# Optimization experiments

Measured on AMD Instinct MI355X. Metric: run time of the kernel, lower is better.

## Reference

```python
import jax, jax.numpy as jnp
import numpy as np
from jax import lax

EPS = 1e-5
B, T, IN, H, D = 16, 512, 128, 256, 8


def setup_inputs() -> dict:
    key = jax.random.key(0)
    ks = jax.random.split(key, 9)
    s = 0.05  # small init to keep tanh unsaturated
    f32 = jnp.float32
    return {
        "y": jax.random.normal(ks[0], (B, T, IN), f32),
        "W_ih": jax.random.normal(ks[1], (H, IN), f32) * s,
        "W_hh": jax.random.normal(ks[2], (H, H), f32) * s,
        "b_ih": jax.random.normal(ks[3], (H,), f32) * s,
        "b_hh": jax.random.normal(ks[4], (H,), f32) * s,
        "W_mean": jax.random.normal(ks[5], (D, H), f32) * s,
        "b_mean": jax.random.normal(ks[6], (D,), f32) * s,
        "W_bd": jax.random.normal(ks[7], (2 * D, H), f32) * s,
        "b_bd": jax.random.normal(ks[8], (2 * D,), f32) * s,
    }


def _forward(y, W_ih, W_hh, b_ih, b_hh, W_mean, b_mean, W_bd, b_bd):
    # --- single-layer unidirectional tanh RNN (torch nn.RNN, batch_first) ---
    x_proj = jnp.einsum("bti,hi->bth", y, W_ih) + b_ih  # [B,T,H]

    def step(h, xt):
        h_new = jnp.tanh(xt + h @ W_hh.T + b_hh)
        return h_new, h_new

    h0 = jnp.zeros((y.shape[0], W_hh.shape[0]), y.dtype)
    _, hs = lax.scan(step, h0, jnp.swapaxes(x_proj, 0, 1))  # [T,B,H]
    enc = jnp.swapaxes(hs, 0, 1)  # [B,T,H]

    mean = enc @ W_mean.T + b_mean  # [B,T,D]
    bd = enc @ W_bd.T + b_bd        # [B,T,2D]

    d = mean.shape[-1]
    t = bd.shape[1]
    diag_e = bd[:, :, :d]        # [B,T,D]  main-diag factor elems
    off_e = bd[:, :-1, d:]       # [B,T-1,D] super-diag factor elems

    a2 = diag_e ** 2
    b2 = jnp.concatenate([jnp.zeros_like(off_e[:, :1]), off_e ** 2], axis=1)  # [B,T,D]
    ab = diag_e[:, :-1] * off_e  # [B,T-1,D]

    main = jnp.swapaxes(a2 + b2, 1, 2) + EPS  # [B,D,T]  (eps*I folded into diag)
    supd = jnp.swapaxes(ab, 1, 2)             # [B,D,T-1]

    i = jnp.arange(t)
    j = jnp.arange(t - 1)
    prec = jnp.zeros((bd.shape[0], d, t, t), bd.dtype)  # [B,D,T,T]
    prec = prec.at[:, :, i, i].set(main)
    prec = prec.at[:, :, j, j + 1].set(supd)
    prec = prec.at[:, :, j + 1, j].set(supd)
    return mean, prec


def reference(y, W_ih, W_hh, b_ih, b_hh, W_mean, b_mean, W_bd, b_bd):
    # Returns the parameters of the D per-dim MultivariateNormal posteriors:
    # mean [B,T,D] and tridiagonal precision matrices [B,D,T,T].
    return _forward(y, W_ih, W_hh, b_ih, b_hh, W_mean, b_mean, W_bd, b_bd)
```

## Files before the change

### kernel.cpp

```cpp
#include <hip/hip_runtime.h>
#include <math.h>

#define BB 16
#define TT 512
#define IND 128
#define HH 256
#define DD 8
#define EPSF 1e-5f

typedef _Float16 h2_t __attribute__((ext_vector_type(2)));

__device__ __forceinline__ float fast_tanh(float x) {
    x = fminf(fmaxf(x, -15.f), 15.f);
    const float e = __expf(2.f * x);
    return __fdividef(e - 1.f, e + 1.f);
}

__device__ __forceinline__ float dpp_xor1(float x) {
    int i = __builtin_bit_cast(int, x);
    i = __builtin_amdgcn_update_dpp(i, i, 0xB1, 0xF, 0xF, true);
    return __builtin_bit_cast(float, i);
}
__device__ __forceinline__ float dpp_xor2(float x) {
    int i = __builtin_bit_cast(int, x);
    i = __builtin_amdgcn_update_dpp(i, i, 0x4E, 0xF, 0xF, true);
    return __builtin_bit_cast(float, i);
}

__global__ __launch_bounds__(512, 4) void xproj_kernel(
    const float* __restrict__ y, const float* __restrict__ W_ih,
    const float* __restrict__ b_ih, const float* __restrict__ b_hh,
    float* __restrict__ xp)
{
    __shared__ __align__(16) float ylds[IND];
    const int tid = threadIdx.x;
    const int j = tid >> 1;
    const int k4 = (tid & 1) * 4;

    float4 w[16];
    const float* wr = W_ih + (size_t)j * IND + k4;
#pragma unroll
    for (int i = 0; i < 16; ++i) w[i] = *(const float4*)(wr + i * 8);
#pragma unroll
    for (int i = 0; i < 16; ++i)
        asm volatile("" : "+v"(w[i].x), "+v"(w[i].y), "+v"(w[i].z), "+v"(w[i].w));
    const float bias = b_ih[j] + b_hh[j];

    const int row0 = blockIdx.x * 16;
    for (int r = 0; r < 16; ++r) {
        const int row = row0 + r;
        if (tid < IND / 4) ((float4*)ylds)[tid] = ((const float4*)(y + (size_t)row * IND))[tid];
        __syncthreads();
        float a0 = 0.f, a1 = 0.f, a2 = 0.f, a3 = 0.f;
#pragma unroll
        for (int i = 0; i < 16; ++i) {
            const float4 hv = *(const float4*)(ylds + i * 8 + k4);
            a0 = fmaf(hv.x, w[i].x, a0);
            a1 = fmaf(hv.y, w[i].y, a1);
            a2 = fmaf(hv.z, w[i].z, a2);
            a3 = fmaf(hv.w, w[i].w, a3);
        }
        float acc = (a0 + a1) + (a2 + a3);
        acc += __shfl_xor(acc, 1);
        if ((tid & 1) == 0) xp[(size_t)row * HH + j] = acc + bias;
        __syncthreads();
    }
}

__global__ __launch_bounds__(256, 2) void scan_fill_kernel(
    const float* __restrict__ xp, const float* __restrict__ W_hh,
    float* __restrict__ enc, float* __restrict__ prec)
{
    if (blockIdx.x >= BB) {
        const size_t n4 = (size_t)BB * DD * TT * TT / 4;
        const float4 z = make_float4(0.f, 0.f, 0.f, 0.f);
        float4* p4 = (float4*)prec;
        size_t idx = (size_t)(blockIdx.x - BB) * blockDim.x + threadIdx.x;
        const size_t stride = (size_t)(gridDim.x - BB) * blockDim.x;
        for (; idx < n4; idx += stride) p4[idx] = z;
        return;
    }

    const int b = blockIdx.x;
    const int tid = threadIdx.x;
    const int j0 = tid >> 2;
    const int k  = tid & 3;
    const int jw = j0 + 64 * k;

    __shared__ __align__(16) char hbufA[4 * 144];
    __shared__ __align__(16) char hbufB[4 * 144];

    h2_t w[4][32];
#pragma unroll
    for (int m = 0; m < 4; ++m) {
        const float* wr = W_hh + (size_t)(j0 + 64 * m) * HH + (size_t)k * 64;
#pragma unroll
        for (int q = 0; q < 16; ++q) {
            const float4 f = ((const float4*)wr)[q];
            h2_t v0; v0.x = (_Float16)f.x; v0.y = (_Float16)f.y;
            h2_t v1; v1.x = (_Float16)f.z; v1.y = (_Float16)f.w;
            w[m][2 * q]     = v0;
            w[m][2 * q + 1] = v1;
        }
    }
#pragma unroll
    for (int m = 0; m < 4; ++m)
#pragma unroll
        for (int i = 0; i < 32; ++i) {
            int tmp = __builtin_bit_cast(int, w[m][i]);
            asm volatile("" : "+v"(tmp));
            w[m][i] = __builtin_bit_cast(h2_t, tmp);
        }

    if (tid < 128) {
        const int m = 2 * tid;
        h2_t z; z.x = (_Float16)0.f; z.y = (_Float16)0.f;
        *(h2_t*)(hbufA + (m >> 6) * 144 + (m & 63) * 2) = z;
    }

    const float* xpb = xp + (size_t)b * TT * HH;
    float* encb = enc + (size_t)b * TT * HH;

    float xbuf[4];
#pragma unroll
    for (int s = 0; s < 4; ++s) xbuf[s] = xpb[(size_t)s * HH + jw];

    __syncthreads();

    const char* hrd = hbufA;
    char* hwr = hbufB;

    for (int tb = 0; tb < TT; tb += 4) {
#pragma unroll
        for (int s = 0; s < 4; ++s) {
            const int t = tb + s;
            const float xc = xbuf[s];
            {
                const int tp = (t + 4 < TT) ? (t + 4) : (TT - 1);
                xbuf[s] = xpb[(size_t)tp * HH + jw];
            }

            float a0 = 0.f, a1 = 0.f, a2 = 0.f, a3 = 0.f;
            const float4* hp = (const float4*)(hrd + k * 144);
#pragma unroll
            for (int i = 0; i < 8; ++i) {
                union { float4 f4; h2_t h[4]; } u;
                u.f4 = hp[i];
#pragma unroll
                for (int q = 0; q < 4; ++q) {
                    a0 = __builtin_amdgcn_fdot2(u.h[q], w[0][4 * i + q], a0, false);
                    a1 = __builtin_amdgcn_fdot2(u.h[q], w[1][4 * i + q], a1, false);
                    a2 = __builtin_amdgcn_fdot2(u.h[q], w[2][4 * i + q], a2, false);
                    a3 = __builtin_amdgcn_fdot2(u.h[q], w[3][4 * i + q], a3, false);
                }
            }
            a0 += dpp_xor1(a0); a0 += dpp_xor2(a0);
            a1 += dpp_xor1(a1); a1 += dpp_xor2(a1);
            a2 += dpp_xor1(a2); a2 += dpp_xor2(a2);
            a3 += dpp_xor1(a3); a3 += dpp_xor2(a3);
            const float p = (k & 1) ? ((k & 2) ? a3 : a1) : ((k & 2) ? a2 : a0);
            const float hn = fast_tanh(xc + p);

            encb[(size_t)t * HH + jw] = hn;
            *(_Float16*)(hwr + k * 144 + j0 * 2) = (_Float16)hn;

            asm volatile("s_waitcnt lgkmcnt(0)\n\ts_barrier" ::: "memory");
            const char* tmp = hrd; hrd = hwr; hwr = (char*)tmp;
        }
    }
}

__global__ __launch_bounds__(256) void head_kernel(
    const float* __restrict__ enc,
    const float* __restrict__ W_mean, const float* __restrict__ b_mean,
    const float* __restrict__ W_bd, const float* __restrict__ b_bd,
    float* __restrict__ mean_out, float* __restrict__ prec)
{
    const int b = blockIdx.x >> 6;
    const int t0 = (blockIdx.x & 63) * 8;
    __shared__ __align__(16) float erow[9][HH];
    __shared__ float vals[8][32];

    const int tid = threadIdx.x;
    {
        const float4* src = (const float4*)(enc + ((size_t)b * TT + t0) * HH - HH);
        float4* dst = (float4*)erow;
        for (int i = tid; i < 9 * (HH / 4); i += 256) dst[i] = src[i];
    }

    const int g = tid >> 3, m = tid & 7;
    const float* wrow;
    float bias;
    if (g < 8)       { wrow = W_mean + (size_t)g * HH;      bias = b_mean[g]; }
    else if (g < 24) { wrow = W_bd + (size_t)(g - 8) * HH;  bias = b_bd[g - 8]; }
    else             { wrow = W_bd + (size_t)(g - 16) * HH; bias = b_bd[g - 16]; }

    float4 wv[8];
#pragma unroll
    for (int i = 0; i < 8; ++i) wv[i] = ((const float4*)wrow)[m * 8 + i];

    __syncthreads();

    for (int r = 0; r < 8; ++r) {
        const float* src = (g >= 24) ? erow[r] : erow[r + 1];
        float acc = 0.f;
#pragma unroll
        for (int i = 0; i < 8; ++i) {
            const float4 hv = ((const float4*)src)[m * 8 + i];
            acc += wv[i].x * hv.x + wv[i].y * hv.y + wv[i].z * hv.z + wv[i].w * hv.w;
        }
        acc += __shfl_xor(acc, 1);
        acc += __shfl_xor(acc, 2);
        acc += __shfl_xor(acc, 4);
        if (m == 0) vals[r][g] = acc + bias;
    }
    __syncthreads();

    const int r = tid >> 5, s = tid & 31;
    const int t = t0 + r;
    if (s < DD) {
        mean_out[((size_t)b * TT + t) * DD + s] = vals[r][s];
    } else if (s < 2 * DD) {
        const int d = s - DD;
        const float diag = vals[r][8 + d];
        const float off  = vals[r][16 + d];
        const float offp = (t > 0) ? vals[r][24 + d] : 0.f;
        const size_t rowbase = (((size_t)b * DD + d) * TT + t) * TT;
        prec[rowbase + t] = diag * diag + offp * offp + EPSF;
        if (t < TT - 1) {
            const float sv = diag * off;
            prec[rowbase + t + 1] = sv;
            prec[(((size_t)b * DD + d) * TT + (t + 1)) * TT + t] = sv;
        }
    }
}

extern "C" void kernel_launch(void* const* d_in, const int* in_sizes, int n_in,
                              void* d_out, int out_size, void* d_ws, size_t ws_size,
                              hipStream_t stream) {
    const float* y      = (const float*)d_in[0];
    const float* W_ih   = (const float*)d_in[1];
    const float* W_hh   = (const float*)d_in[2];
    const float* b_ih   = (const float*)d_in[3];
    const float* b_hh   = (const float*)d_in[4];
    const float* W_mean = (const float*)d_in[5];
    const float* b_mean = (const float*)d_in[6];
    const float* W_bd   = (const float*)d_in[7];
    const float* b_bd   = (const float*)d_in[8];

    float* out  = (float*)d_out;
    float* mean = out;
    float* prec = out + (size_t)BB * TT * DD;

    float* xp  = (float*)d_ws;
    float* enc = xp + (size_t)BB * TT * HH;

    xproj_kernel<<<512, 512, 0, stream>>>(y, W_ih, b_ih, b_hh, xp);
    scan_fill_kernel<<<1008, 256, 0, stream>>>(xp, W_hh, enc, prec);
    head_kernel<<<1024, 256, 0, stream>>>(enc, W_mean, b_mean, W_bd, b_bd, mean, prec);
}
```

Measured before the change: 410.9 us.

## Split recurrent matvec across 8 lanes per row group with 512-thread scan blocks

The sequential RNN scan block grows from 256 to 512 threads. Each output group's K=256 reduction is now split across 8 lanes instead of 4, which halves the per-thread fdot2 chain and the register-resident W_hh slice, and adds a cross-lane shfl_xor(4) stage to the reduction. Only half the lanes write results. The fill blocks also become 512 threads, doubling the zeroing parallelism. The cost is a barrier across 8 waves instead of 4 per timestep, plus the extra shuffle latency on the critical path.

```diff
diff --git a/kernel.cpp b/kernel.cpp
--- a/kernel.cpp
+++ b/kernel.cpp
@@ -9,6 +9,7 @@
 #define EPSF 1e-5f
 
 typedef _Float16 h2_t __attribute__((ext_vector_type(2)));
+typedef float f32x4 __attribute__((ext_vector_type(4)));
 
 __device__ __forceinline__ float fast_tanh(float x) {
     x = fminf(fmaxf(x, -15.f), 15.f);
@@ -67,46 +68,47 @@
     }
 }
 
-__global__ __launch_bounds__(256, 2) void scan_fill_kernel(
+__global__ __launch_bounds__(512, 2) void scan_fill_kernel(
     const float* __restrict__ xp, const float* __restrict__ W_hh,
     float* __restrict__ enc, float* __restrict__ prec)
 {
     if (blockIdx.x >= BB) {
         const size_t n4 = (size_t)BB * DD * TT * TT / 4;
-        const float4 z = make_float4(0.f, 0.f, 0.f, 0.f);
-        float4* p4 = (float4*)prec;
+        const f32x4 z = {0.f, 0.f, 0.f, 0.f};
+        f32x4* p4 = (f32x4*)prec;
         size_t idx = (size_t)(blockIdx.x - BB) * blockDim.x + threadIdx.x;
         const size_t stride = (size_t)(gridDim.x - BB) * blockDim.x;
         for (; idx < n4; idx += stride) p4[idx] = z;
         return;
     }
 
-    const int b = blockIdx.x;
+    const int b   = blockIdx.x;
     const int tid = threadIdx.x;
-    const int j0 = tid >> 2;
-    const int k  = tid & 3;
-    const int jw = j0 + 64 * k;
+    const int g   = tid >> 3;
+    const int k   = tid & 7;
+    const int kk  = k & 3;
+    const int jw  = g + 64 * kk;
+    const bool act = (k < 4);
 
     __shared__ __align__(16) char hbufA[4 * 144];
     __shared__ __align__(16) char hbufB[4 * 144];
 
-    h2_t w[4][32];
+    h2_t w[4][16];
 #pragma unroll
     for (int m = 0; m < 4; ++m) {
-        const float* wr = W_hh + (size_t)(j0 + 64 * m) * HH + (size_t)k * 64;
-#pragma unroll
-        for (int q = 0; q < 16; ++q) {
-            const float4 f = ((const float4*)wr)[q];
-            h2_t v0; v0.x = (_Float16)f.x; v0.y = (_Float16)f.y;
-            h2_t v1; v1.x = (_Float16)f.z; v1.y = (_Float16)f.w;
-            w[m][2 * q]     = v0;
-            w[m][2 * q + 1] = v1;
+        const float* wr = W_hh + (size_t)(g + 64 * m) * HH + (size_t)k * 32;
+#pragma unroll
+        for (int i = 0; i < 16; ++i) {
+            h2_t v;
+            v.x = (_Float16)wr[2 * i];
+            v.y = (_Float16)wr[2 * i + 1];
+            w[m][i] = v;
         }
     }
 #pragma unroll
     for (int m = 0; m < 4; ++m)
 #pragma unroll
-        for (int i = 0; i < 32; ++i) {
+        for (int i = 0; i < 16; ++i) {
             int tmp = __builtin_bit_cast(int, w[m][i]);
             asm volatile("" : "+v"(tmp));
             w[m][i] = __builtin_bit_cast(h2_t, tmp);
@@ -118,8 +120,8 @@
         *(h2_t*)(hbufA + (m >> 6) * 144 + (m & 63) * 2) = z;
     }
 
-    const float* xpb = xp + (size_t)b * TT * HH;
-    float* encb = enc + (size_t)b * TT * HH;
+    const float* xpb  = xp  + (size_t)b * TT * HH;
+    float*       encb = enc + (size_t)b * TT * HH;
 
     float xbuf[4];
 #pragma unroll
@@ -130,44 +132,47 @@
     const char* hrd = hbufA;
     char* hwr = hbufB;
 
+#define SCAN_STEP(TSTEP, S)                                                       \
+    {                                                                             \
+        const int t_ = (TSTEP);                                                   \
+        const float xc = xbuf[S];                                                 \
+        const int tp_ = (t_ + 4 < TT) ? t_ + 4 : TT - 1;                          \
+        xbuf[S] = xpb[(size_t)tp_ * HH + jw];                                     \
+        float a0 = 0.f, a1 = 0.f, a2 = 0.f, a3 = 0.f;                             \
+        const float4* hp = (const float4*)(hrd + (k >> 1) * 144 + (k & 1) * 64);  \
+        _Pragma("unroll")                                                         \
+        for (int i = 0; i < 4; ++i) {                                             \
+            union { float4 f4; h2_t h[4]; } u;                                    \
+            u.f4 = hp[i];                                                         \
+            _Pragma("unroll")                                                     \
+            for (int e = 0; e < 4; ++e) {                                         \
+                a0 = __builtin_amdgcn_fdot2(u.h[e], w[0][4 * i + e], a0, false);  \
+                a1 = __builtin_amdgcn_fdot2(u.h[e], w[1][4 * i + e], a1, false);  \
+                a2 = __builtin_amdgcn_fdot2(u.h[e], w[2][4 * i + e], a2, false);  \
+                a3 = __builtin_amdgcn_fdot2(u.h[e], w[3][4 * i + e], a3, false);  \
+            }                                                                     \
+        }                                                                         \
+        a0 += dpp_xor1(a0); a0 += dpp_xor2(a0); a0 += __shfl_xor(a0, 4);          \
+        a1 += dpp_xor1(a1); a1 += dpp_xor2(a1); a1 += __shfl_xor(a1, 4);          \
+        a2 += dpp_xor1(a2); a2 += dpp_xor2(a2); a2 += __shfl_xor(a2, 4);          \
+        a3 += dpp_xor1(a3); a3 += dpp_xor2(a3); a3 += __shfl_xor(a3, 4);          \
+        const float p = (kk & 1) ? ((kk & 2) ? a3 : a1) : ((kk & 2) ? a2 : a0);   \
+        const float hn = fast_tanh(xc + p);                                       \
+        if (act) {                                                                \
+            encb[(size_t)t_ * HH + jw] = hn;                                      \
+            *(_Float16*)(hwr + kk * 144 + g * 2) = (_Float16)hn;                  \
+        }                                                                         \
+        asm volatile("s_waitcnt lgkmcnt(0)\n\ts_barrier" ::: "memory");           \
+        { const char* tmp_ = hrd; hrd = hwr; hwr = (char*)tmp_; }                 \
+    }
+
     for (int tb = 0; tb < TT; tb += 4) {
-#pragma unroll
-        for (int s = 0; s < 4; ++s) {
-            const int t = tb + s;
-            const float xc = xbuf[s];
-            {
-                const int tp = (t + 4 < TT) ? (t + 4) : (TT - 1);
-                xbuf[s] = xpb[(size_t)tp * HH + jw];
-            }
-
-            float a0 = 0.f, a1 = 0.f, a2 = 0.f, a3 = 0.f;
-            const float4* hp = (const float4*)(hrd + k * 144);
-#pragma unroll
-            for (int i = 0; i < 8; ++i) {
-                union { float4 f4; h2_t h[4]; } u;
-                u.f4 = hp[i];
-#pragma unroll
-                for (int q = 0; q < 4; ++q) {
-                    a0 = __builtin_amdgcn_fdot2(u.h[q], w[0][4 * i + q], a0, false);
-                    a1 = __builtin_amdgcn_fdot2(u.h[q], w[1][4 * i + q], a1, false);
-                    a2 = __builtin_amdgcn_fdot2(u.h[q], w[2][4 * i + q], a2, false);
-                    a3 = __builtin_amdgcn_fdot2(u.h[q], w[3][4 * i + q], a3, false);
-                }
-            }
-            a0 += dpp_xor1(a0); a0 += dpp_xor2(a0);
-            a1 += dpp_xor1(a1); a1 += dpp_xor2(a1);
-            a2 += dpp_xor1(a2); a2 += dpp_xor2(a2);
-            a3 += dpp_xor1(a3); a3 += dpp_xor2(a3);
-            const float p = (k & 1) ? ((k & 2) ? a3 : a1) : ((k & 2) ? a2 : a0);
-            const float hn = fast_tanh(xc + p);
-
-            encb[(size_t)t * HH + jw] = hn;
-            *(_Float16*)(hwr + k * 144 + j0 * 2) = (_Float16)hn;
-
-            asm volatile("s_waitcnt lgkmcnt(0)\n\ts_barrier" ::: "memory");
-            const char* tmp = hrd; hrd = hwr; hwr = (char*)tmp;
-        }
-    }
+        SCAN_STEP(tb,     0)
+        SCAN_STEP(tb + 1, 1)
+        SCAN_STEP(tb + 2, 2)
+        SCAN_STEP(tb + 3, 3)
+    }
+#undef SCAN_STEP
 }
 
 __global__ __launch_bounds__(256) void head_kernel(
@@ -256,6 +261,6 @@
     float* enc = xp + (size_t)BB * TT * HH;
 
     xproj_kernel<<<512, 512, 0, stream>>>(y, W_ih, b_ih, b_hh, xp);
-    scan_fill_kernel<<<1008, 256, 0, stream>>>(xp, W_hh, enc, prec);
+    scan_fill_kernel<<<1008, 512, 0, stream>>>(xp, W_hh, enc, prec);
     head_kernel<<<1024, 256, 0, stream>>>(enc, W_mean, b_mean, W_bd, b_bd, mean, prec);
 }
```

New measurement: 459.5 us. 11.8% more time.
